# Kernel tuning notes

Measured on AMD Instinct MI355X. Metric: run time of the kernel, lower is better.

## Reference

```python
import jax, jax.numpy as jnp
import numpy as np

N_VARS = 2048
D_GRAPH = 256
NUM_ADJ = 7
ALPHA = 0.9
MASK = 0.5


def setup_inputs() -> dict:
    key = jax.random.key(0)
    ks = jax.random.split(key, 8)
    init_adj = jax.random.uniform(ks[0], (N_VARS, N_VARS), dtype=jnp.float32, minval=-1.0, maxval=1.0)
    emb1 = jax.random.normal(ks[1], (NUM_ADJ, N_VARS, D_GRAPH), dtype=jnp.float32)
    emb2 = jax.random.normal(ks[2], (NUM_ADJ, N_VARS, D_GRAPH), dtype=jnp.float32)
    lim = 1.0 / np.sqrt(D_GRAPH)
    w1 = jax.random.uniform(ks[3], (NUM_ADJ, D_GRAPH, D_GRAPH), dtype=jnp.float32, minval=-lim, maxval=lim)
    b1 = jax.random.uniform(ks[4], (NUM_ADJ, D_GRAPH), dtype=jnp.float32, minval=-lim, maxval=lim)
    w2 = jax.random.uniform(ks[5], (NUM_ADJ, D_GRAPH, D_GRAPH), dtype=jnp.float32, minval=-lim, maxval=lim)
    b2 = jax.random.uniform(ks[6], (NUM_ADJ, D_GRAPH), dtype=jnp.float32, minval=-lim, maxval=lim)
    time_indices = jax.random.randint(ks[7], (8,), 0, NUM_ADJ)
    return {
        'init_adj': init_adj, 'emb1': emb1, 'emb2': emb2,
        'w1': w1, 'b1': b1, 'w2': w2, 'b2': b2,
        'time_indices': time_indices, 'current_epoch': 10,
    }


def reference(init_adj, emb1, emb2, w1, b1, w2, b2, time_indices, current_epoch):
    n = init_adj.shape[0]
    k = int(n * n * MASK)
    prop = min(current_epoch / 5, ALPHA)  # static python scalar schedule
    eye = jnp.eye(n, dtype=init_adj.dtype)

    def build_one(e1, e2, W1, B1, W2, B2):
        # nn.Linear: x @ W.T + b, then tanh
        nv1 = jnp.tanh(e1 @ W1.T + B1)          # [n, d]
        nv2 = jnp.tanh(e2 @ W2.T + B2)          # [n, d]
        a = (1.0 - prop) * init_adj + prop * (nv1 @ nv2.T)  # [n, n]
        adj = jax.nn.relu(jnp.tanh(a))
        adj = adj * (1.0 - eye)                 # remove diagonal
        flat = adj.reshape(-1)
        _, idx = jax.lax.top_k(flat, k)         # data-dependent sparsification
        m = jnp.zeros_like(flat).at[idx].set(1.0)
        adj = m.reshape(n, n) * adj
        adj = adj + eye
        return adj / adj.sum(axis=1, keepdims=True)  # row-degree normalize

    oadj = jax.vmap(build_one)(emb1, emb2, w1, b1, w2, b2)  # [num_adj, n, n]
    return oadj[time_indices]  # [B, n, n]
```

## Files before the change

### kernel.cpp

```cpp
#include <hip/hip_runtime.h>
#include <cstdint>
#include <cstddef>

#define NVARS 2048
#define DG    256
#define NSLOT 8
#define NN2   (NVARS*NVARS)
#define K_SEL 2097152u
#define CAP   (1u<<18)
#define KS    512

typedef __attribute__((ext_vector_type(8))) short short8;
typedef __attribute__((ext_vector_type(8))) unsigned short ushort8;
typedef __attribute__((ext_vector_type(4))) float floatx4;

__device__ __align__(16) unsigned short g_ebig[NSLOT][2][NVARS*KS];
__device__ __align__(16) unsigned short g_wbig[NSLOT][2][DG*KS];
__device__ __align__(16) unsigned short g_abig[NSLOT][NVARS*KS];
__device__ __align__(16) unsigned short g_bbig[NSLOT][NVARS*KS];
__device__ unsigned g_hist[NSLOT][2048];
__device__ unsigned g_cand[NSLOT][CAP];
__device__ unsigned g_state[NSLOT][16];
__device__ float g_scal[2];

__device__ __forceinline__ unsigned fkey(float x){
  unsigned b = __float_as_uint(x);
  return (b & 0x80000000u) ? ~b : (b | 0x80000000u);
}
__device__ __forceinline__ unsigned short f2bf(float v){
  unsigned u = __float_as_uint(v);
  return (unsigned short)((u + 0x7FFFu + ((u >> 16) & 1u)) >> 16);
}
__device__ __forceinline__ void async16(void* lds, const void* g){
  __builtin_amdgcn_global_load_lds(
      (const __attribute__((address_space(1))) unsigned int*)g,
      (__attribute__((address_space(3))) unsigned int*)lds, 16, 0, 0);
}

__global__ __launch_bounds__(256) void k_prep(const int* __restrict__ tind,
                                              const int* __restrict__ epoch_p){
  int tid = threadIdx.x;
  if (tid < NSLOT){
    int t = tind[tid];
    int fo = tid;
    for (int b = 0; b < tid; b++){ if (tind[b] == t){ fo = b; break; } }
    g_state[tid][0] = (fo == tid) ? 1u : 0u;
    g_state[tid][1] = (unsigned)fo;
    g_state[tid][2] = 0u;
    g_state[tid][3] = K_SEL;
    g_state[tid][4] = 0u;
    g_state[tid][7] = 0x7FFFFFFFu;
    g_state[tid][8] = 0u;
  }
  if (tid == 0){
    double pd = (double)epoch_p[0] / 5.0;
    if (pd > 0.9) pd = 0.9;
    g_scal[0] = (float)(1.0 - pd);
    g_scal[1] = (float)pd;
  }
  unsigned* h = (unsigned*)g_hist;
  for (int i = tid; i < NSLOT*2048; i += 256) h[i] = 0u;
}

__global__ __launch_bounds__(256) void k_split(
    const float* __restrict__ emb1, const float* __restrict__ emb2,
    const float* __restrict__ w1,  const float* __restrict__ w2,
    const int* __restrict__ tind){
  int z = blockIdx.z; int s = z >> 1; int side = z & 1;
  if (!g_state[s][0]) return;
  int t = tind[s];
  int flat = blockIdx.x*256 + threadIdx.x;
  const float* src;
  unsigned short* dst;
  if (flat < 65536){
    int row = flat >> 5, g8 = flat & 31;
    src = (side ? emb2 : emb1) + (size_t)t*NVARS*DG + (size_t)row*DG + g8*8;
    dst = g_ebig[s][side] + (size_t)row*KS + g8*8;
  } else {
    int f2 = flat - 65536;
    int row = f2 >> 5, g8 = f2 & 31;
    src = (side ? w2 : w1) + (size_t)t*DG*DG + (size_t)row*DG + g8*8;
    dst = g_wbig[s][side] + (size_t)row*KS + g8*8;
  }
  float4 v0 = *(const float4*)src;
  float4 v1 = *(const float4*)(src + 4);
  float a[8] = {v0.x,v0.y,v0.z,v0.w,v1.x,v1.y,v1.z,v1.w};
  ushort8 hi8, lo8;
  #pragma unroll
  for (int j = 0; j < 8; j++){
    unsigned short hb = f2bf(a[j]);
    float hv = __uint_as_float(((unsigned)hb) << 16);
    hi8[j] = hb;
    lo8[j] = f2bf(a[j] - hv);
  }
  *(ushort8*)dst         = hi8;
  *(ushort8*)(dst + 256) = lo8;
}

__global__ __launch_bounds__(256, 2) void k_gemm_nv(
    const float* __restrict__ b1, const float* __restrict__ b2,
    const int* __restrict__ tind){
  int z = blockIdx.z; int s = z >> 1; int side = z & 1;
  if (!g_state[s][0]) return;
  int t = tind[s];
  const unsigned short* __restrict__ A = g_ebig[s][side];
  const unsigned short* __restrict__ B = g_wbig[s][side];
  const float* __restrict__ bias = (side ? b2 : b1) + (size_t)t*DG;
  unsigned short* __restrict__ dst = side ? g_bbig[s] : g_abig[s];
  __shared__ __align__(16) unsigned short As[128*64];
  __shared__ __align__(16) unsigned short Bs[128*64];
  __shared__ __align__(16) float Cs[128][68];
  int tid = threadIdx.x;
  int lane = tid & 63, wv = tid >> 6;
  int rowBase = blockIdx.y*128, colBase = blockIdx.x*128;
  int rW = (wv >> 1)*64, cW = (wv & 1)*64;
  int m = lane & 15, q = lane >> 4;
  int rl = lane >> 3, sl = lane & 7;
  floatx4 acc[4][4] = {};
  for (int p = 0; p < 3; p++){
    int aoff = (p == 1) ? 256 : 0;
    int boff = (p == 2) ? 256 : 0;
    for (int k0 = 0; k0 < 256; k0 += 64){
      #pragma unroll
      for (int t4 = 0; t4 < 4; t4++){
        int rloc = wv*32 + t4*8 + rl;
        int g = sl ^ (rloc & 7);
        async16(&As[(wv*32 + t4*8)*64], A + (size_t)(rowBase + rloc)*KS + aoff + k0 + g*8);
        async16(&Bs[(wv*32 + t4*8)*64], B + (size_t)(colBase + rloc)*KS + boff + k0 + g*8);
      }
      __syncthreads();
      #pragma unroll
      for (int kk = 0; kk < 2; kk++){
        short8 af[4], bfr[4];
        #pragma unroll
        for (int i = 0; i < 4; i++){
          int rA = rW + i*16 + m;
          af[i]  = *(const short8*)&As[rA*64 + (((kk*4 + q) ^ (rA & 7))*8)];
          int rB = cW + i*16 + m;
          bfr[i] = *(const short8*)&Bs[rB*64 + (((kk*4 + q) ^ (rB & 7))*8)];
        }
        #pragma unroll
        for (int i = 0; i < 4; i++)
          #pragma unroll
          for (int j = 0; j < 4; j++)
            acc[i][j] = __builtin_amdgcn_mfma_f32_16x16x32_bf16(af[i], bfr[j], acc[i][j], 0, 0, 0);
      }
      __syncthreads();
    }
  }
  for (int h = 0; h < 2; h++){
    if ((wv & 1) == h){
      #pragma unroll
      for (int i = 0; i < 4; i++)
        #pragma unroll
        for (int j = 0; j < 4; j++)
          #pragma unroll
          for (int r = 0; r < 4; r++)
            Cs[rW + i*16 + q*4 + r][j*16 + m] = acc[i][j][r];
    }
    __syncthreads();
    #pragma unroll
    for (int it = 0; it < 4; it++){
      int row = it*32 + (tid >> 3);
      int c8  = (tid & 7)*8;
      float4 va = *(const float4*)&Cs[row][c8];
      float4 vb = *(const float4*)&Cs[row][c8 + 4];
      float v[8] = {va.x,va.y,va.z,va.w,vb.x,vb.y,vb.z,vb.w};
      int colb = colBase + h*64 + c8;
      ushort8 hi8, lo8;
      #pragma unroll
      for (int j = 0; j < 8; j++){
        float e = tanhf(v[j] + bias[colb + j]);
        unsigned short hb = f2bf(e);
        float hv = __uint_as_float(((unsigned)hb) << 16);
        hi8[j] = hb;
        lo8[j] = f2bf(e - hv);
      }
      unsigned short* rp = dst + (size_t)(rowBase + row)*KS;
      *(ushort8*)(rp + colb)       = hi8;
      *(ushort8*)(rp + 256 + colb) = lo8;
    }
    __syncthreads();
  }
}

__global__ __launch_bounds__(256, 2) void k_gemm_s(const float* __restrict__ init,
                                                   float* __restrict__ out){
  int s = blockIdx.z;
  if (!g_state[s][0]) return;
  const unsigned short* __restrict__ A = g_abig[s];
  const unsigned short* __restrict__ B = g_bbig[s];
  __shared__ __align__(16) unsigned short SM[2][128*128];
  __shared__ unsigned hloc[2048];
  unsigned short* As = SM[0];
  unsigned short* Bs = SM[1];
  int tid = threadIdx.x;
  int lane = tid & 63, wv = tid >> 6;
  int rowBase = blockIdx.y*128, colBase = blockIdx.x*128;
  int rW = (wv >> 1)*64, cW = (wv & 1)*64;
  int m = lane & 15, q = lane >> 4;
  int rl4 = lane >> 4;
  int gl  = lane & 15;
  for (int i = tid; i < 2048; i += 256) hloc[i] = 0u;
  floatx4 acc[4][4] = {};
  for (int k0 = 0; k0 < 256; k0 += 64){
    #pragma unroll
    for (int t8 = 0; t8 < 8; t8++){
      int rloc = wv*32 + t8*4 + rl4;
      int g = (gl & 8) | ((gl ^ rloc) & 7);
      int off = ((g & 8) ? 256 : 0) + k0 + (g & 7)*8;
      async16(&As[(wv*32 + t8*4)*128], A + (size_t)(rowBase + rloc)*KS + off);
      async16(&Bs[(wv*32 + t8*4)*128], B + (size_t)(colBase + rloc)*KS + off);
    }
    __syncthreads();
    #pragma unroll
    for (int kk = 0; kk < 2; kk++){
      short8 ah[4], bh[4], al[4], bl[4];
      #pragma unroll
      for (int i = 0; i < 4; i++){
        int rA = rW + i*16 + m;
        int pa = (kk*4 + q) ^ (rA & 7);
        ah[i] = *(const short8*)&As[rA*128 + pa*8];
        al[i] = *(const short8*)&As[rA*128 + (8 + pa)*8];
        int rB = cW + i*16 + m;
        int pb = (kk*4 + q) ^ (rB & 7);
        bh[i] = *(const short8*)&Bs[rB*128 + pb*8];
        bl[i] = *(const short8*)&Bs[rB*128 + (8 + pb)*8];
      }
      #pragma unroll
      for (int i = 0; i < 4; i++)
        #pragma unroll
        for (int j = 0; j < 4; j++){
          acc[i][j] = __builtin_amdgcn_mfma_f32_16x16x32_bf16(ah[i], bh[j], acc[i][j], 0, 0, 0);
          acc[i][j] = __builtin_amdgcn_mfma_f32_16x16x32_bf16(al[i], bh[j], acc[i][j], 0, 0, 0);
          acc[i][j] = __builtin_amdgcn_mfma_f32_16x16x32_bf16(ah[i], bl[j], acc[i][j], 0, 0, 0);
        }
    }
    __syncthreads();
  }
  float am1 = g_scal[0], am2 = g_scal[1];
  float* __restrict__ outs = out + (size_t)s*NN2;
  float (*Cs)[68] = (float(*)[68])SM;
  for (int h = 0; h < 2; h++){
    if ((wv & 1) == h){
      #pragma unroll
      for (int i = 0; i < 4; i++)
        #pragma unroll
        for (int j = 0; j < 4; j++)
          #pragma unroll
          for (int r = 0; r < 4; r++)
            Cs[rW + i*16 + q*4 + r][j*16 + m] = acc[i][j][r];
    }
    __syncthreads();
    #pragma unroll
    for (int it = 0; it < 4; it++){
      int row = it*32 + (tid >> 3);
      int c8  = (tid & 7)*8;
      float4 va = *(const float4*)&Cs[row][c8];
      float4 vb = *(const float4*)&Cs[row][c8 + 4];
      float v[8] = {va.x,va.y,va.z,va.w,vb.x,vb.y,vb.z,vb.w};
      int grow = rowBase + row;
      int col  = colBase + h*64 + c8;
      const float* ip = init + (size_t)grow*NVARS + col;
      float4 i0 = *(const float4*)ip;
      float4 i1 = *(const float4*)(ip + 4);
      float iv[8] = {i0.x,i0.y,i0.z,i0.w,i1.x,i1.y,i1.z,i1.w};
      float o[8];
      #pragma unroll
      for (int j = 0; j < 8; j++){
        float val = am1*iv[j] + am2*v[j];
        if (grow == col + j) val = -__builtin_inff();
        o[j] = val;
        atomicAdd(&hloc[fkey(val) >> 21], 1u);
      }
      float* op = outs + (size_t)grow*NVARS + col;
      *(float4*)op       = make_float4(o[0], o[1], o[2], o[3]);
      *(float4*)(op + 4) = make_float4(o[4], o[5], o[6], o[7]);
    }
    __syncthreads();
  }
  for (int i = tid; i < 2048; i += 256){
    unsigned c = hloc[i];
    if (c) atomicAdd(&g_hist[s][i], c);
  }
}

__device__ void desc_select(unsigned* h, unsigned* sc, int nb, unsigned rank,
                            unsigned* od, unsigned* orem, unsigned* ocnt){
  int tid = threadIdx.x;
  int per = nb >> 8;
  unsigned loc[8];
  unsigned own = 0;
  int base = tid*per;
  for (int j = 0; j < per; j++){ loc[j] = h[base+j]; own += loc[j]; }
  sc[tid] = own;
  __syncthreads();
  for (int off = 1; off < 256; off <<= 1){
    unsigned v = (tid + off < 256) ? sc[tid+off] : 0u;
    __syncthreads();
    sc[tid] += v;
    __syncthreads();
  }
  unsigned acc = sc[tid] - own;
  for (int j = per-1; j >= 0; j--){
    unsigned c = loc[j];
    if (c && rank > acc && rank <= acc + c){ *od = (unsigned)(base+j); *orem = rank - acc; *ocnt = c; }
    acc += c;
  }
  __syncthreads();
}
__device__ void asc_select(unsigned* h, unsigned* sc, int nb, unsigned rank,
                           unsigned* od, unsigned* orem){
  int tid = threadIdx.x;
  int per = nb >> 8;
  unsigned loc[8];
  unsigned own = 0;
  int base = tid*per;
  for (int j = 0; j < per; j++){ loc[j] = h[base+j]; own += loc[j]; }
  sc[tid] = own;
  __syncthreads();
  for (int off = 1; off < 256; off <<= 1){
    unsigned v = (tid >= off) ? sc[tid-off] : 0u;
    __syncthreads();
    sc[tid] += v;
    __syncthreads();
  }
  unsigned below = sc[tid] - own;
  for (int j = 0; j < per; j++){
    unsigned c = loc[j];
    if (c && rank > below && rank <= below + c){ *od = (unsigned)(base+j); *orem = rank - below; }
    below += c;
  }
  __syncthreads();
}

__global__ __launch_bounds__(256) void k_select1(){
  int s = blockIdx.x;
  if (!g_state[s][0]) return;
  int tid = threadIdx.x;
  __shared__ unsigned h[2048];
  __shared__ unsigned sc[256];
  __shared__ unsigned sd, srem, scnt;
  for (int i = tid; i < 2048; i += 256) h[i] = g_hist[s][i];
  if (tid == 0){ sd = 0; srem = 1; scnt = 1; }
  __syncthreads();
  desc_select(h, sc, 2048, K_SEL, &sd, &srem, &scnt);
  if (tid == 0){ g_state[s][2] = sd << 21; g_state[s][3] = srem; }
}

__global__ __launch_bounds__(256) void k_collect(const float* __restrict__ out){
  int s = blockIdx.z;
  if (!g_state[s][0]) return;
  unsigned pb = g_state[s][2] >> 21;
  const float4* p = (const float4*)(out + (size_t)s*NN2);
  int stride = gridDim.x*256;
  for (int i = blockIdx.x*256 + threadIdx.x; i < NN2/4; i += stride){
    float4 v = p[i];
    float xs[4] = {v.x, v.y, v.z, v.w};
    #pragma unroll
    for (int j = 0; j < 4; j++){
      if ((fkey(xs[j]) >> 21) == pb){
        unsigned pos = atomicAdd(&g_state[s][8], 1u);
        if (pos < CAP) g_cand[s][pos] = (unsigned)(i*4 + j);
      }
    }
  }
}

__global__ __launch_bounds__(256) void k_final(const float* __restrict__ out){
  int s = blockIdx.x;
  if (!g_state[s][0]) return;
  int tid = threadIdx.x;
  unsigned mcnt = g_state[s][8]; if (mcnt > CAP) mcnt = CAP;
  unsigned krem = g_state[s][3];
  unsigned prefix = g_state[s][2];
  const float* outs = out + (size_t)s*NN2;
  __shared__ unsigned h[2048];
  __shared__ unsigned sc[256];
  __shared__ unsigned sd, srem, scnt;
  for (int i = tid; i < 2048; i += 256) h[i] = 0u;
  if (tid == 0){ sd = 0; srem = 1; scnt = 1; }
  __syncthreads();
  for (unsigned i = tid; i < mcnt; i += 256){
    unsigned u = fkey(outs[g_cand[s][i]]);
    atomicAdd(&h[(u >> 10) & 0x7FFu], 1u);
  }
  __syncthreads();
  desc_select(h, sc, 2048, krem, &sd, &srem, &scnt);
  unsigned d1 = sd, krem2 = srem;
  __syncthreads();
  for (int i = tid; i < 2048; i += 256) h[i] = 0u;
  __syncthreads();
  for (unsigned i = tid; i < mcnt; i += 256){
    unsigned u = fkey(outs[g_cand[s][i]]);
    if (((u >> 10) & 0x7FFu) == d1) atomicAdd(&h[u & 0x3FFu], 1u);
  }
  __syncthreads();
  desc_select(h, sc, 1024, krem2, &sd, &srem, &scnt);
  unsigned d0 = sd, nek = srem, cnteq = scnt;
  __syncthreads();
  unsigned tu = prefix | (d1 << 10) | d0;
  unsigned cutoff = 0x7FFFFFFFu;
  if (nek < cnteq){
    for (int i = tid; i < 2048; i += 256) h[i] = 0u;
    __syncthreads();
    for (unsigned i = tid; i < mcnt; i += 256){
      unsigned idx = g_cand[s][i];
      if (fkey(outs[idx]) == tu) atomicAdd(&h[idx >> 11], 1u);
    }
    __syncthreads();
    asc_select(h, sc, 2048, nek, &sd, &srem);
    unsigned dh = sd, j2 = srem;
    __syncthreads();
    for (int i = tid; i < 2048; i += 256) h[i] = 0u;
    __syncthreads();
    for (unsigned i = tid; i < mcnt; i += 256){
      unsigned idx = g_cand[s][i];
      if (fkey(outs[idx]) == tu && (idx >> 11) == dh) atomicAdd(&h[idx & 0x7FFu], 1u);
    }
    __syncthreads();
    asc_select(h, sc, 2048, j2, &sd, &srem);
    cutoff = (dh << 11) | sd;
    __syncthreads();
  }
  if (tid == 0){ g_state[s][4] = tu; g_state[s][7] = cutoff; }
}

__global__ __launch_bounds__(256) void k_masknorm(float* __restrict__ out){
  int s = blockIdx.y;
  if (!g_state[s][0]) return;
  int r = blockIdx.x;
  int tid = threadIdx.x;
  unsigned tu = g_state[s][4];
  unsigned cutoff = g_state[s][7];
  const float4* rowp = (const float4*)(out + (size_t)s*NN2 + (size_t)r*NVARS);
  unsigned baseIdx = (unsigned)(r*NVARS);
  float4 res[2];
  double lsum = 0.0;
  #pragma unroll
  for (int t = 0; t < 2; t++){
    int c4 = tid + t*256;
    float4 a4 = rowp[c4];
    float av[4] = {a4.x, a4.y, a4.z, a4.w};
    float rv[4];
    #pragma unroll
    for (int j = 0; j < 4; j++){
      int c = c4*4 + j;
      float vv;
      if (c == r) vv = 1.0f;
      else {
        unsigned u = fkey(av[j]);
        bool keep = (u > tu) || (u == tu && (baseIdx + (unsigned)c) <= cutoff);
        vv = keep ? fmaxf(tanhf(av[j]), 0.0f) : 0.0f;
      }
      rv[j] = vv;
      lsum += (double)vv;
    }
    res[t].x = rv[0]; res[t].y = rv[1]; res[t].z = rv[2]; res[t].w = rv[3];
  }
  __shared__ double red[256];
  red[tid] = lsum;
  __syncthreads();
  for (int off = 128; off > 0; off >>= 1){
    if (tid < off) red[tid] += red[tid+off];
    __syncthreads();
  }
  float inv = 1.0f / (float)red[0];
  #pragma unroll
  for (int t = 0; t < 2; t++){
    res[t].x *= inv; res[t].y *= inv; res[t].z *= inv; res[t].w *= inv;
  }
  for (int s2 = 0; s2 < NSLOT; s2++){
    if (g_state[s2][1] == (unsigned)s){
      float4* dst = (float4*)(out + (size_t)s2*NN2 + (size_t)r*NVARS);
      dst[tid]       = res[0];
      dst[tid + 256] = res[1];
    }
  }
}

extern "C" void kernel_launch(void* const* d_in, const int* in_sizes, int n_in,
                              void* d_out, int out_size, void* d_ws, size_t ws_size,
                              hipStream_t stream){
  (void)in_sizes; (void)n_in; (void)d_ws; (void)ws_size; (void)out_size;
  const float* init = (const float*)d_in[0];
  const float* emb1 = (const float*)d_in[1];
  const float* emb2 = (const float*)d_in[2];
  const float* w1   = (const float*)d_in[3];
  const float* b1   = (const float*)d_in[4];
  const float* w2   = (const float*)d_in[5];
  const float* b2   = (const float*)d_in[6];
  const int* tind   = (const int*)d_in[7];
  const int* epoch  = (const int*)d_in[8];
  float* out = (float*)d_out;

  k_prep<<<1, 256, 0, stream>>>(tind, epoch);
  k_split<<<dim3(288, 1, 16), 256, 0, stream>>>(emb1, emb2, w1, w2, tind);
  k_gemm_nv<<<dim3(2, 16, 16), 256, 0, stream>>>(b1, b2, tind);
  k_gemm_s<<<dim3(16, 16, 8), 256, 0, stream>>>(init, out);
  k_select1<<<8, 256, 0, stream>>>();
  k_collect<<<dim3(256, 1, 8), 256, 0, stream>>>(out);
  k_final<<<8, 256, 0, stream>>>(out);
  k_masknorm<<<dim3(2048, 8), 256, 0, stream>>>(out);
}
```

Measured before the change: 346.5 us.

## Double-buffer split-bf16 GEMM tiles and restructure K loop into 12 phases

The split-bf16 (hi/lo) GEMM is restructured from four 64-wide K steps, each doing three MFMAs per tile pair, into twelve 64-wide phases (hi*hi, lo*hi, hi*lo), each doing one MFMA per pair. Shared memory is reorganised into two ping-pong buffers of 128x64 tiles, so the next phase's async loads are issued before computing the current one, overlapping global loads with MFMA and removing one barrier per step. In exchange, each phase streams a fresh A and B tile, which raises global/LDS traffic and MFMA-to-load ratio shifts.

```diff
diff --git a/kernel.cpp b/kernel.cpp
--- a/kernel.cpp
+++ b/kernel.cpp
@@ -190,54 +190,59 @@
   if (!g_state[s][0]) return;
   const unsigned short* __restrict__ A = g_abig[s];
   const unsigned short* __restrict__ B = g_bbig[s];
-  __shared__ __align__(16) unsigned short SM[2][128*128];
+  __shared__ __align__(16) unsigned short SM[4][128*64];
   __shared__ unsigned hloc[2048];
-  unsigned short* As = SM[0];
-  unsigned short* Bs = SM[1];
   int tid = threadIdx.x;
   int lane = tid & 63, wv = tid >> 6;
   int rowBase = blockIdx.y*128, colBase = blockIdx.x*128;
   int rW = (wv >> 1)*64, cW = (wv & 1)*64;
   int m = lane & 15, q = lane >> 4;
-  int rl4 = lane >> 4;
-  int gl  = lane & 15;
+  int rl = lane >> 3, sl = lane & 7;
   for (int i = tid; i < 2048; i += 256) hloc[i] = 0u;
   floatx4 acc[4][4] = {};
-  for (int k0 = 0; k0 < 256; k0 += 64){
+
+  auto stage = [&](int kt, int b){
+    int phase = kt >> 2;
+    int within = (kt & 3) * 64;
+    int aoff = ((phase == 1) ? 256 : 0) + within;
+    int boff = ((phase == 2) ? 256 : 0) + within;
+    unsigned short* As = SM[2*b];
+    unsigned short* Bs = SM[2*b + 1];
     #pragma unroll
-    for (int t8 = 0; t8 < 8; t8++){
-      int rloc = wv*32 + t8*4 + rl4;
-      int g = (gl & 8) | ((gl ^ rloc) & 7);
-      int off = ((g & 8) ? 256 : 0) + k0 + (g & 7)*8;
-      async16(&As[(wv*32 + t8*4)*128], A + (size_t)(rowBase + rloc)*KS + off);
-      async16(&Bs[(wv*32 + t8*4)*128], B + (size_t)(colBase + rloc)*KS + off);
-    }
-    __syncthreads();
+    for (int t4 = 0; t4 < 4; t4++){
+      int rloc = wv*32 + t4*8 + rl;
+      int g = sl ^ (rloc & 7);
+      async16(&As[(wv*32 + t4*8)*64], A + (size_t)(rowBase + rloc)*KS + aoff + g*8);
+      async16(&Bs[(wv*32 + t4*8)*64], B + (size_t)(colBase + rloc)*KS + boff + g*8);
+    }
+  };
+
+  stage(0, 0);
+  __syncthreads();
+  for (int kt = 0; kt < 12; kt++){
+    int b = kt & 1;
+    if (kt < 11) stage(kt + 1, b ^ 1);
+    const unsigned short* As = SM[2*b];
+    const unsigned short* Bs = SM[2*b + 1];
     #pragma unroll
     for (int kk = 0; kk < 2; kk++){
-      short8 ah[4], bh[4], al[4], bl[4];
+      short8 af[4], bfr[4];
       #pragma unroll
       for (int i = 0; i < 4; i++){
         int rA = rW + i*16 + m;
-        int pa = (kk*4 + q) ^ (rA & 7);
-        ah[i] = *(const short8*)&As[rA*128 + pa*8];
-        al[i] = *(const short8*)&As[rA*128 + (8 + pa)*8];
+        af[i]  = *(const short8*)&As[rA*64 + (((kk*4 + q) ^ (rA & 7))*8)];
         int rB = cW + i*16 + m;
-        int pb = (kk*4 + q) ^ (rB & 7);
-        bh[i] = *(const short8*)&Bs[rB*128 + pb*8];
-        bl[i] = *(const short8*)&Bs[rB*128 + (8 + pb)*8];
+        bfr[i] = *(const short8*)&Bs[rB*64 + (((kk*4 + q) ^ (rB & 7))*8)];
       }
       #pragma unroll
       for (int i = 0; i < 4; i++)
         #pragma unroll
-        for (int j = 0; j < 4; j++){
-          acc[i][j] = __builtin_amdgcn_mfma_f32_16x16x32_bf16(ah[i], bh[j], acc[i][j], 0, 0, 0);
-          acc[i][j] = __builtin_amdgcn_mfma_f32_16x16x32_bf16(al[i], bh[j], acc[i][j], 0, 0, 0);
-          acc[i][j] = __builtin_amdgcn_mfma_f32_16x16x32_bf16(ah[i], bl[j], acc[i][j], 0, 0, 0);
-        }
-    }
-    __syncthreads();
-  }
+        for (int j = 0; j < 4; j++)
+          acc[i][j] = __builtin_amdgcn_mfma_f32_16x16x32_bf16(af[i], bfr[j], acc[i][j], 0, 0, 0);
+    }
+    __syncthreads();
+  }
+
   float am1 = g_scal[0], am2 = g_scal[1];
   float* __restrict__ outs = out + (size_t)s*NN2;
   float (*Cs)[68] = (float(*)[68])SM;
```

Result: slower. 358.1 us (+3.3%).
